# Kernel tuning notes

Measured on AMD Instinct MI355X. Metric: run time of the kernel, lower is better.

## Reference

```python
import jax, jax.numpy as jnp
import numpy as np

K = 3  # kernel_size; stride=1, padding=1 so num_D=D, num_H=H, num_W=W


def _neighborhood_diff(x):
    """For each voxel, (center - each of its 27 zero-padded 3x3x3 neighbors).

    Equivalent to F.interpolate(x, scale_factor=3, 'nearest') - overlap_expand3D(x)
    reshaped to [B, C, D, 3, H, 3, W, 3]: out[..., d, kd, h, kh, w, kw] =
    x[d,h,w] - x_pad[d+kd, h+kh, w+kw].
    """
    B, C, D, H, W = x.shape
    xp = jnp.pad(x, ((0, 0), (0, 0), (1, 1), (1, 1), (1, 1)))
    # gather shifted copies along each spatial dim (27 static slices)
    p = jnp.stack([xp[:, :, kd:kd + D] for kd in range(K)], axis=3)            # B,C,D,3,H+2,W+2
    p = jnp.stack([p[:, :, :, :, kh:kh + H] for kh in range(K)], axis=5)       # B,C,D,3,H,3,W+2
    p = jnp.stack([p[..., kw:kw + W] for kw in range(K)], axis=7)              # B,C,D,3,H,3,W,3
    center = x[:, :, :, None, :, None, :, None]                                # nearest-upsample, factored
    return center - p


def setup_inputs() -> dict:
    key = jax.random.key(0)
    k1, k2 = jax.random.split(key)
    shape = (2, 1, 32, 128, 128)  # B, C, D, H, W
    x = jax.random.normal(k1, shape, dtype=jnp.float32)
    y = jax.random.normal(k2, shape, dtype=jnp.float32)
    return {"x": x, "y": y}


def reference(x, y):
    x_diff = _neighborhood_diff(x)
    y_diff = _neighborhood_diff(y)
    return jnp.mean(jnp.abs(x_diff - y_diff))
```

## Files before the change

### kernel.cpp

```cpp
#include <hip/hip_runtime.h>

constexpr int Dd = 32, Hh = 128, Ww = 128, Bv = 2;
constexpr int NVOX = Bv * Dd * Hh * Ww;
constexpr int BLK  = 512;
constexpr int BLKF = 256;

constexpr int TD = 2, TH = 4;
constexpr int ZT = Dd / TD;
constexpr int YT = Hh / TH;
constexpr int NBLK = Bv * ZT * YT;
constexpr int LSTR = 136;
constexpr int RZ = TD + 1, RY = TH + 2;
constexpr int NROWS = RZ * RY;
constexpr int NF2   = LSTR / 2;
constexpr int NITEM = NROWS * NF2;

__device__ __constant__ const signed char DIRZ[13] = {1,1,1, 1,1,1, 1,1,1, 0,0,0, 0};
__device__ __constant__ const signed char DIRY[13] = {-1,-1,-1, 0,0,0, 1,1,1, 1,1,1, 0};
__device__ __constant__ const signed char DIRW[13] = {-1,0,1, -1,0,1, -1,0,1, -1,0,1, 1};

__global__ void __launch_bounds__(BLK, 8)
cdl_worker(const float* __restrict__ xg, const float* __restrict__ yg,
           float* __restrict__ partials)
{
    __shared__ float lds[NROWS * LSTR];
    __shared__ float smem[BLK / 64];

    const int tid = threadIdx.x;
    const int bid = (blockIdx.x & 7) * (NBLK / 8) + (blockIdx.x >> 3);

    int t = bid;
    const int yt  = t & (YT - 1); t >>= 5;
    const int zt  = t & (ZT - 1); t >>= 4;
    const int vol = t;
    const int z0 = zt * TD, y0 = yt * TH;
    const size_t vbase = (size_t)vol * Dd * Hh * Ww;

#pragma unroll
    for (int p = 0; p < 3; ++p) {
        const int idx = p * BLK + tid;
        if (idx < NITEM) {
            const int row  = idx / NF2;
            const int slot = idx - row * NF2;
            const int lzr  = row / RY;
            const int lyr  = row - lzr * RY;
            const int gz = z0 + lzr;
            const int gy = y0 + lyr - 1;
            const int w  = 2 * slot - 4;
            float2 v = make_float2(0.f, 0.f);
            if ((unsigned)gz < (unsigned)Dd && (unsigned)gy < (unsigned)Hh &&
                (unsigned)w <= 126u) {
                const size_t g = vbase + ((size_t)gz * Hh + gy) * Ww + w;
                const float2 a = *(const float2*)(xg + g);
                const float2 b = *(const float2*)(yg + g);
                v = make_float2(a.x - b.x, a.y - b.y);
            }
            *(float2*)&lds[row * LSTR + 2 * slot] = v;
        }
    }
    __syncthreads();

    const int j  = tid & 63;
    const int r  = tid >> 6;
    const int lz = r >> 2;
    const int ly = r & 3;
    const int k0 = 2 * j + 4;

    const float2 c = *(const float2*)&lds[(lz * RY + ly + 1) * LSTR + k0];

    float sp = 0.f;
    {
        const float Qx = lds[(lz * RY + ly + 1) * LSTR + k0 + 2];
        sp += fabsf(c.x - c.y) + fabsf(c.y - Qx);
    }
#define ROW6(RP) do { const float* rp_ = (RP);                              \
        const float2 M = *(const float2*)&rp_[k0 - 2];                      \
        const float2 A = *(const float2*)&rp_[k0];                          \
        const float2 Q = *(const float2*)&rp_[k0 + 2];                      \
        sp += fabsf(c.x - M.y) + fabsf(c.x - A.x) + fabsf(c.x - A.y);       \
        sp += fabsf(c.y - A.x) + fabsf(c.y - A.y) + fabsf(c.y - Q.x);      \
    } while (0)
    ROW6(&lds[(lz * RY + ly + 2) * LSTR]);
    ROW6(&lds[((lz + 1) * RY + ly    ) * LSTR]);
    ROW6(&lds[((lz + 1) * RY + ly + 1) * LSTR]);
    ROW6(&lds[((lz + 1) * RY + ly + 2) * LSTR]);
#undef ROW6

    const int gz = z0 + lz, gy = y0 + ly;
    const bool zl = (gz == 0), zh = (gz == Dd - 1);
    const bool yl = (gy == 0), yh = (gy == Hh - 1);
    const bool wlx = (j == 0);
    const bool why = (j == 63);
    int ndx = 0, ndy = 0;
#pragma unroll
    for (int q = 0; q < 13; ++q) {
        const int oz = DIRZ[q], oy = DIRY[q], ow = DIRW[q];
        const bool bpx = (oz > 0 && zh) || (oy > 0 && yh) || (oy < 0 && yl)
                       || (ow < 0 && wlx);
        const bool bmx = (oz > 0 && zl) || (oy > 0 && yl) || (oy < 0 && yh)
                       || (ow > 0 && wlx);
        const bool bpy = (oz > 0 && zh) || (oy > 0 && yh) || (oy < 0 && yl)
                       || (ow > 0 && why);
        const bool bmy = (oz > 0 && zl) || (oy > 0 && yl) || (oy < 0 && yh)
                       || (ow < 0 && why);
        ndx += (int)bmx - (int)bpx;
        ndy += (int)bmy - (int)bpy;
    }

    float s = 2.f * sp + fabsf(c.x) * (float)ndx + fabsf(c.y) * (float)ndy;

    const int lane = tid & 63;
    const int wid  = tid >> 6;
#pragma unroll
    for (int off = 32; off > 0; off >>= 1) s += __shfl_down(s, off, 64);
    if (lane == 0) smem[wid] = s;
    __syncthreads();
    if (tid == 0) {
        float tsum = 0.f;
#pragma unroll
        for (int w = 0; w < BLK / 64; ++w) tsum += smem[w];
        partials[bid] = tsum;
    }
}

__global__ void __launch_bounds__(BLKF)
cdl_finish(const float* __restrict__ partials, float* __restrict__ out)
{
    float acc = 0.f;
#pragma unroll
    for (int i = 0; i < NBLK / BLKF; ++i)
        acc += partials[i * BLKF + threadIdx.x];
#pragma unroll
    for (int off = 32; off > 0; off >>= 1) acc += __shfl_down(acc, off, 64);

    __shared__ float smem[BLKF / 64];
    const int lane = threadIdx.x & 63;
    const int wid  = threadIdx.x >> 6;
    if (lane == 0) smem[wid] = acc;
    __syncthreads();
    if (threadIdx.x == 0) {
        const double tot = (double)smem[0] + (double)smem[1] +
                           (double)smem[2] + (double)smem[3];
        out[0] = (float)(tot / (27.0 * (double)NVOX));
    }
}

extern "C" void kernel_launch(void* const* d_in, const int* in_sizes, int n_in,
                              void* d_out, int out_size, void* d_ws, size_t ws_size,
                              hipStream_t stream) {
    const float* x  = (const float*)d_in[0];
    const float* y  = (const float*)d_in[1];
    float* partials = (float*)d_ws;
    float* out      = (float*)d_out;

    cdl_worker<<<NBLK, BLK, 0, stream>>>(x, y, partials);
    cdl_finish<<<1, BLKF, 0, stream>>>(partials, out);
}
```

Measured before the change: 11.49 us.

## Double z-tile depth per block and widen staging loads to float4

Each block now covers four z-planes instead of two, and every thread handles two output rows. This cuts the share of halo rows loaded into LDS and halves the number of blocks and partials. The global-to-LDS staging moves from float2 to float4 loads, so fewer load instructions are issued. In exchange the grid has half as many blocks, launch bounds drop to four waves per SIMD, and more registers are used per thread, which may lower parallelism on a small problem.

Result: slower. 11.86 us (+3.2%).

```diff
diff --git a/kernel.cpp b/kernel.cpp
--- a/kernel.cpp
+++ b/kernel.cpp
@@ -5,21 +5,21 @@
 constexpr int BLK  = 512;
 constexpr int BLKF = 256;
 
-constexpr int TD = 2, TH = 4;
+constexpr int TD = 4, TH = 4;
 constexpr int ZT = Dd / TD;
 constexpr int YT = Hh / TH;
 constexpr int NBLK = Bv * ZT * YT;
 constexpr int LSTR = 136;
 constexpr int RZ = TD + 1, RY = TH + 2;
 constexpr int NROWS = RZ * RY;
-constexpr int NF2   = LSTR / 2;
-constexpr int NITEM = NROWS * NF2;
+constexpr int NF4   = LSTR / 4;
+constexpr int NITEM = NROWS * NF4;
 
 __device__ __constant__ const signed char DIRZ[13] = {1,1,1, 1,1,1, 1,1,1, 0,0,0, 0};
 __device__ __constant__ const signed char DIRY[13] = {-1,-1,-1, 0,0,0, 1,1,1, 1,1,1, 0};
 __device__ __constant__ const signed char DIRW[13] = {-1,0,1, -1,0,1, -1,0,1, -1,0,1, 1};
 
-__global__ void __launch_bounds__(BLK, 8)
+__global__ void __launch_bounds__(BLK, 4)
 cdl_worker(const float* __restrict__ xg, const float* __restrict__ yg,
            float* __restrict__ partials)
 {
@@ -31,48 +31,55 @@
 
     int t = bid;
     const int yt  = t & (YT - 1); t >>= 5;
-    const int zt  = t & (ZT - 1); t >>= 4;
+    const int zt  = t & (ZT - 1); t >>= 3;
     const int vol = t;
     const int z0 = zt * TD, y0 = yt * TH;
     const size_t vbase = (size_t)vol * Dd * Hh * Ww;
 
 #pragma unroll
-    for (int p = 0; p < 3; ++p) {
+    for (int p = 0; p < 2; ++p) {
         const int idx = p * BLK + tid;
         if (idx < NITEM) {
-            const int row  = idx / NF2;
-            const int slot = idx - row * NF2;
+            const int row  = idx / NF4;
+            const int slot = idx - row * NF4;
             const int lzr  = row / RY;
             const int lyr  = row - lzr * RY;
             const int gz = z0 + lzr;
             const int gy = y0 + lyr - 1;
-            const int w  = 2 * slot - 4;
-            float2 v = make_float2(0.f, 0.f);
+            const int w  = 4 * slot - 4;
+            float4 v = make_float4(0.f, 0.f, 0.f, 0.f);
             if ((unsigned)gz < (unsigned)Dd && (unsigned)gy < (unsigned)Hh &&
-                (unsigned)w <= 126u) {
+                (unsigned)w < (unsigned)Ww) {
                 const size_t g = vbase + ((size_t)gz * Hh + gy) * Ww + w;
-                const float2 a = *(const float2*)(xg + g);
-                const float2 b = *(const float2*)(yg + g);
-                v = make_float2(a.x - b.x, a.y - b.y);
+                const float4 a = *(const float4*)(xg + g);
+                const float4 b = *(const float4*)(yg + g);
+                v = make_float4(a.x - b.x, a.y - b.y, a.z - b.z, a.w - b.w);
             }
-            *(float2*)&lds[row * LSTR + 2 * slot] = v;
+            *(float4*)&lds[row * LSTR + 4 * slot] = v;
         }
     }
     __syncthreads();
 
-    const int j  = tid & 63;
-    const int r  = tid >> 6;
-    const int lz = r >> 2;
-    const int ly = r & 3;
+    const int j = tid & 63;
+    const int r = tid >> 6;
     const int k0 = 2 * j + 4;
+    const bool wlx = (j == 0);
+    const bool why = (j == 63);
 
-    const float2 c = *(const float2*)&lds[(lz * RY + ly + 1) * LSTR + k0];
+    float s = 0.f;
+#pragma unroll
+    for (int q = 0; q < 2; ++q) {
+        const int rr = r * 2 + q;
+        const int lz = rr >> 2;
+        const int ly = rr & 3;
 
-    float sp = 0.f;
-    {
-        const float Qx = lds[(lz * RY + ly + 1) * LSTR + k0 + 2];
-        sp += fabsf(c.x - c.y) + fabsf(c.y - Qx);
-    }
+        const float2 c = *(const float2*)&lds[(lz * RY + ly + 1) * LSTR + k0];
+
+        float sp = 0.f;
+        {
+            const float Qx = lds[(lz * RY + ly + 1) * LSTR + k0 + 2];
+            sp += fabsf(c.x - c.y) + fabsf(c.y - Qx);
+        }
 #define ROW6(RP) do { const float* rp_ = (RP);                              \
         const float2 M = *(const float2*)&rp_[k0 - 2];                      \
         const float2 A = *(const float2*)&rp_[k0];                          \
@@ -80,34 +87,33 @@
         sp += fabsf(c.x - M.y) + fabsf(c.x - A.x) + fabsf(c.x - A.y);       \
         sp += fabsf(c.y - A.x) + fabsf(c.y - A.y) + fabsf(c.y - Q.x);      \
     } while (0)
-    ROW6(&lds[(lz * RY + ly + 2) * LSTR]);
-    ROW6(&lds[((lz + 1) * RY + ly    ) * LSTR]);
-    ROW6(&lds[((lz + 1) * RY + ly + 1) * LSTR]);
-    ROW6(&lds[((lz + 1) * RY + ly + 2) * LSTR]);
+        ROW6(&lds[(lz * RY + ly + 2) * LSTR]);
+        ROW6(&lds[((lz + 1) * RY + ly    ) * LSTR]);
+        ROW6(&lds[((lz + 1) * RY + ly + 1) * LSTR]);
+        ROW6(&lds[((lz + 1) * RY + ly + 2) * LSTR]);
 #undef ROW6
 
-    const int gz = z0 + lz, gy = y0 + ly;
-    const bool zl = (gz == 0), zh = (gz == Dd - 1);
-    const bool yl = (gy == 0), yh = (gy == Hh - 1);
-    const bool wlx = (j == 0);
-    const bool why = (j == 63);
-    int ndx = 0, ndy = 0;
+        const int gz = z0 + lz, gy = y0 + ly;
+        const bool zl = (gz == 0), zh = (gz == Dd - 1);
+        const bool yl = (gy == 0), yh = (gy == Hh - 1);
+        int ndx = 0, ndy = 0;
 #pragma unroll
-    for (int q = 0; q < 13; ++q) {
-        const int oz = DIRZ[q], oy = DIRY[q], ow = DIRW[q];
-        const bool bpx = (oz > 0 && zh) || (oy > 0 && yh) || (oy < 0 && yl)
-                       || (ow < 0 && wlx);
-        const bool bmx = (oz > 0 && zl) || (oy > 0 && yl) || (oy < 0 && yh)
-                       || (ow > 0 && wlx);
-        const bool bpy = (oz > 0 && zh) || (oy > 0 && yh) || (oy < 0 && yl)
-                       || (ow > 0 && why);
-        const bool bmy = (oz > 0 && zl) || (oy > 0 && yl) || (oy < 0 && yh)
-                       || (ow < 0 && why);
-        ndx += (int)bmx - (int)bpx;
-        ndy += (int)bmy - (int)bpy;
+        for (int qd = 0; qd < 13; ++qd) {
+            const int oz = DIRZ[qd], oy = DIRY[qd], ow = DIRW[qd];
+            const bool bpx = (oz > 0 && zh) || (oy > 0 && yh) || (oy < 0 && yl)
+                           || (ow < 0 && wlx);
+            const bool bmx = (oz > 0 && zl) || (oy > 0 && yl) || (oy < 0 && yh)
+                           || (ow > 0 && wlx);
+            const bool bpy = (oz > 0 && zh) || (oy > 0 && yh) || (oy < 0 && yl)
+                           || (ow > 0 && why);
+            const bool bmy = (oz > 0 && zl) || (oy > 0 && yl) || (oy < 0 && yh)
+                           || (ow < 0 && why);
+            ndx += (int)bmx - (int)bpx;
+            ndy += (int)bmy - (int)bpy;
+        }
+
+        s += 2.f * sp + fabsf(c.x) * (float)ndx + fabsf(c.y) * (float)ndy;
     }
-
-    float s = 2.f * sp + fabsf(c.x) * (float)ndx + fabsf(c.y) * (float)ndy;
 
     const int lane = tid & 63;
     const int wid  = tid >> 6;
```
